# Kernel tuning notes

Measured on AMD Instinct MI355X. Metric: run time of the kernel, lower is better.

The kernel has to match this reference:

```python
import jax, jax.numpy as jnp
import numpy as np

T, B, F, P = 1024, 2048, 11, 256
KAPPA_MAX = 0.1
N_GRID = 100


def setup_inputs() -> dict:
    key = jax.random.key(0)
    k1, k2, k3, k4, k5 = jax.random.split(key, 5)
    aidx = jax.random.randint(k1, (T, B), 0, 2)
    actions = jax.nn.one_hot(aidx, 2, dtype=jnp.float32)            # (T,B,2) one-hot choice
    rewards = jax.random.bernoulli(k2, 0.5, (T, B, 2)).astype(jnp.float32)
    cd_cur = jax.random.uniform(k3, (T, B, 1), minval=-0.1, maxval=0.1)
    cd_next = jax.random.uniform(k4, (T, B, 1), minval=-0.1, maxval=0.1)
    meta = jnp.zeros((T, B, 4), dtype=jnp.float32)                  # timestep/trial/block/experiment (unused)
    pid = jax.random.randint(k5, (B,), 0, P).astype(jnp.float32)
    pid_feat = jnp.broadcast_to(pid[None, :, None], (T, B, 1))
    inputs = jnp.concatenate([actions, rewards, cd_cur, cd_next, meta, pid_feat], axis=-1)
    inputs = inputs[:, None]                                        # (T, 1, B, 11)
    return {
        "inputs": inputs,
        "beta_raw": jnp.zeros((P,), dtype=jnp.float32),
        "sigma_raw": jnp.zeros((P,), dtype=jnp.float32),
    }


def reference(inputs, beta_raw, sigma_raw):
    p_mu = jnp.linspace(0.0, 1.0, N_GRID)                           # (100,)
    x = jnp.nan_to_num(inputs[:, 0])                                # (T, B, 11)
    pid = x[0, :, -1].astype(jnp.int32)                             # (B,)
    beta = jnp.clip(jax.nn.softplus(beta_raw) + 1.0, 1.0, 25.0)[pid]    # (B,)
    sigma = jnp.clip(jax.nn.sigmoid(sigma_raw) * 0.09 + 0.01, 0.01, 0.1)[pid]  # (B,)
    inv_s = 1.0 / (sigma * jnp.sqrt(2.0))

    def ncdf(v, mean):
        return 0.5 * (1.0 + jax.lax.erf((v - mean) * inv_s))

    def state_beliefs(cd):
        u = ncdf(0.0, cd)
        v = ncdf(-KAPPA_MAX, cd)
        w = ncdf(KAPPA_MAX, cd)
        denom = jnp.maximum(w - v, 1e-10)
        pi_0 = jnp.clip((u - v) / denom, 0.0, 1.0)
        pi_1 = jnp.clip((w - u) / denom, 0.0, 1.0)
        return pi_0, pi_1

    def step(belief, x_t):
        acts = x_t[:, :2]
        rews = x_t[:, 2:4]
        cd_current = x_t[:, 4]
        cd_next = x_t[:, 5]
        had_choice = acts.sum(-1) > 0
        action_idx = jnp.argmax(acts, axis=-1)
        reward_scalar = (rews * acts).sum(-1)
        pi_0, pi_1 = state_beliefs(cd_current)
        r = jnp.where(action_idx == 0, reward_scalar, 1.0 - reward_scalar)
        q_0 = pi_1 * r + pi_0 * (1.0 - r)
        q_1 = (2.0 * r - 1.0) * (pi_0 - pi_1)
        update = q_1[:, None] * p_mu + q_0[:, None]                 # (B, 100)
        update = jnp.where(had_choice[:, None], update, 1.0)
        belief = jnp.maximum(belief * update, 1e-30)
        belief_norm = belief / belief.sum(-1, keepdims=True)
        E_mu = (belief_norm * p_mu).sum(-1)                         # (B,)
        pi_0n, pi_1n = state_beliefs(cd_next)
        v_a0 = (pi_0n - pi_1n) * E_mu + pi_1n
        v_a1 = (pi_1n - pi_0n) * E_mu + pi_0n
        logits_t = beta[:, None] * jnp.stack([v_a0, v_a1], axis=-1)  # (B, 2)
        return belief, logits_t

    belief0 = jnp.ones((x.shape[1], N_GRID), dtype=x.dtype)
    belief, logits = jax.lax.scan(step, belief0, x)                 # logits: (T, B, 2)
    logits = logits[:, None]                                        # (T, 1, B, 2)
    return logits, belief
```

## Files before the change

### kernel.cpp

```cpp
#include <hip/hip_runtime.h>
#include <math.h>

#define TT  1024
#define BB  2048
#define FF  11
#define PP  256
#define NG  100
#define NCH 16
#define LCH (TT / NCH)
#define JJ  4

typedef float f32x2 __attribute__((ext_vector_type(2)));

__device__ __forceinline__ float nz(float v) { return (v != v) ? 0.f : v; }

__device__ __forceinline__ float erf_fast(float x) {
    float ax = fabsf(x);
    float t  = __builtin_amdgcn_rcpf(fmaf(0.3275911f, ax, 1.f));
    float y  = fmaf(fmaf(fmaf(fmaf(1.061405429f, t, -1.453152027f), t,
                              1.421413741f), t, -0.284496736f), t, 0.254829592f);
    y *= t;
    float r = fmaf(-y, __expf(-ax * ax), 1.f);
    return copysignf(r, x);
}

__global__ __launch_bounds__(256) void phase1_kernel(
    const float* __restrict__ x, const float* __restrict__ beta_raw,
    const float* __restrict__ sigma_raw, float4* __restrict__ QC)
{
    __shared__ float s[256 * FF];
    const int tid = threadIdx.x;
    const size_t base = (size_t)blockIdx.x * (256 * FF);
    {
        const float4* x4 = (const float4*)(x + base);
        float4* s4 = (float4*)s;
        #pragma unroll
        for (int k = tid; k < 704; k += 256) s4[k] = x4[k];
    }
    __syncthreads();

    const int idx = blockIdx.x * 256 + tid;
    const int b   = idx & (BB - 1);
    const float* rec = s + tid * FF;
    float a0  = nz(rec[0]);
    float a1  = nz(rec[1]);
    float r0  = nz(rec[2]);
    float r1  = nz(rec[3]);
    float cdc = nz(rec[4]);
    float cdn = nz(rec[5]);

    int pid = (int)nz(x[(size_t)b * FF + 10]);
    pid = pid < 0 ? 0 : (pid > PP - 1 ? PP - 1 : pid);
    float br = beta_raw[pid];
    float sr = sigma_raw[pid];
    float sp   = fmaxf(br, 0.f) + log1pf(__expf(-fabsf(br)));
    float beta = fminf(fmaxf(sp + 1.f, 1.f), 25.f);
    float sig  = fminf(fmaxf(__builtin_amdgcn_rcpf(1.f + __expf(-sr)) * 0.09f + 0.01f,
                             0.01f), 0.1f);
    float inv_s = 1.f / (sig * 1.41421356237309505f);

    float u = 0.5f * (1.f + erf_fast((0.0f  - cdc) * inv_s));
    float v = 0.5f * (1.f + erf_fast((-0.1f - cdc) * inv_s));
    float w = 0.5f * (1.f + erf_fast((0.1f  - cdc) * inv_s));
    float inv = 1.f / fmaxf(w - v, 1e-10f);
    float pi0 = fminf(fmaxf((u - v) * inv, 0.f), 1.f);
    float pi1 = fminf(fmaxf((w - u) * inv, 0.f), 1.f);

    u = 0.5f * (1.f + erf_fast((0.0f  - cdn) * inv_s));
    v = 0.5f * (1.f + erf_fast((-0.1f - cdn) * inv_s));
    w = 0.5f * (1.f + erf_fast((0.1f  - cdn) * inv_s));
    inv = 1.f / fmaxf(w - v, 1e-10f);
    float pi0n = fminf(fmaxf((u - v) * inv, 0.f), 1.f);
    float pi1n = fminf(fmaxf((w - u) * inv, 0.f), 1.f);

    float rs = r0 * a0 + r1 * a1;
    float r  = (a0 >= a1) ? rs : 1.f - rs;
    float q0 = pi1 * r + pi0 * (1.f - r);
    float q1 = (2.f * r - 1.f) * (pi0 - pi1);
    if (!((a0 + a1) > 0.f)) { q0 = 1.f; q1 = 0.f; }

    QC[idx] = make_float4(q0, q1, beta * pi1n, beta * pi0n);
}

template <int CTRL, int RMASK>
__device__ __forceinline__ float dpp_add(float v) {
    int t = __builtin_amdgcn_update_dpp(0, __float_as_int(v), CTRL, RMASK, 0xF, true);
    return v + __int_as_float(t);
}
__device__ __forceinline__ float red8(float v) {
    v = dpp_add<0xB1,  0xF>(v);
    v = dpp_add<0x4E,  0xF>(v);
    v = dpp_add<0x141, 0xF>(v);
    return v;
}


__global__ __launch_bounds__(256) void phaseA_kernel(
    const float4* __restrict__ QC, float2* __restrict__ UC)
{
    const int lane = threadIdx.x & 63;
    const int wib  = threadIdx.x >> 6;
    const int W    = blockIdx.x * 4 + wib;
    const int pair = W & 1023;
    const int c    = W >> 10;
    const int lig  = lane & 31;
    const int b    = 2 * pair + (lane >> 5);
    const int t0   = c * LCH;

    const f32x2 p01 = { (float)lig        * (1.f / 99.f),
                        (float)(lig + 32) * (1.f / 99.f) };
    const f32x2 p23 = { (float)(lig + 64) * (1.f / 99.f),
                        (float)(lig + 96) * (1.f / 99.f) };
    const f32x2 cl01 = { 1e-30f, 1e-30f };
    const f32x2 cl23 = { 1e-30f, (lig < 4) ? 1e-30f : 0.f };

    f32x2 U01 = { 1.f, 1.f }, U23 = { 1.f, 1.f };
    f32x2 C01 = { 0.f, 0.f }, C23 = { 0.f, 0.f };

    const char* QCb = (const char*)QC;
    unsigned off = ((unsigned)t0 * BB + (unsigned)b) * 16u;

    float4 pre[JJ];
    #pragma unroll
    for (int j = 0; j < JJ; ++j)
        pre[j] = *(const float4*)(QCb + (off + (unsigned)j * (BB * 16u)));
    off += JJ * (BB * 16u);

    for (int tt = 0; tt < LCH; tt += JJ) {
        #pragma unroll
        for (int j = 0; j < JJ; ++j) {
            float4 q = pre[j];
            pre[j] = *(const float4*)(QCb + (off + (unsigned)j * (BB * 16u)));
            f32x2 qx = { q.x, q.x }, qy = { q.y, q.y };
            f32x2 u01 = qy * p01 + qx;
            f32x2 u23 = qy * p23 + qx;
            U01 *= u01;
            U23 *= u23;
            C01 = __builtin_elementwise_max(C01 * u01, cl01);
            C23 = __builtin_elementwise_max(C23 * u23, cl23);
        }
        off += JJ * (BB * 16u);
    }

    float2* dst = UC + ((size_t)c * BB + b) * NG;
    dst[lig]      = make_float2(U01.x, C01.x);
    dst[lig + 32] = make_float2(U01.y, C01.y);
    dst[lig + 64] = make_float2(U23.x, C23.x);
    if (lig < 4) dst[lig + 96] = make_float2(U23.y, C23.y);
}

__global__ __launch_bounds__(256) void phaseB_kernel(
    const float2* __restrict__ UC, float* __restrict__ BE)
{
    const int flat = blockIdx.x * 256 + threadIdx.x;
    float be = 1.f;
    #pragma unroll
    for (int c = 0; c < NCH; ++c) {
        BE[(size_t)c * (BB * NG) + flat] = be;
        float2 uc = UC[(size_t)c * (BB * NG) + flat];
        be = fmaxf(be * uc.x, uc.y);
    }
}

__global__ __launch_bounds__(256) void phaseC_kernel(
    const float4* __restrict__ QC, const float* __restrict__ BE,
    float* __restrict__ out)
{
    const int lane = threadIdx.x & 63;
    const int wib  = threadIdx.x >> 6;
    const int W    = blockIdx.x * 4 + wib;
    const int wg   = W & 255;
    const int c    = W >> 8;
    const int sl   = lane & 7;
    const int g    = lane >> 3;
    const int b    = wg * 8 + g;
    const int t0   = c * LCH;

    f32x2 p[7];
    #pragma unroll
    for (int k = 0; k < 7; ++k)
        p[k] = (f32x2){ (float)(sl + 16 * k)     * (1.f / 99.f),
                        (float)(sl + 16 * k + 8) * (1.f / 99.f) };
    const f32x2 clA = { 1e-30f, 1e-30f };
    const f32x2 cl6 = { (sl < 4) ? 1e-30f : 0.f, 0.f };

    const float* ebase = BE + (size_t)c * (BB * NG) + (size_t)b * NG;
    f32x2 be[7];
    #pragma unroll
    for (int k = 0; k < 6; ++k)
        be[k] = (f32x2){ ebase[sl + 16 * k], ebase[sl + 16 * k + 8] };
    be[6] = (f32x2){ (sl < 4) ? ebase[sl + 96] : 0.f, 0.f };

    const char* QCb = (const char*)QC;
    char* outb = (char*)out;
    unsigned off  = ((unsigned)t0 * BB + (unsigned)b) * 16u;
    unsigned soff = ((unsigned)t0 * (2 * BB) + 2 * (unsigned)b) * 4u;

    float4 pre[JJ];
    #pragma unroll
    for (int j = 0; j < JJ; ++j)
        pre[j] = *(const float4*)(QCb + (off + (unsigned)j * (BB * 16u)));
    off += JJ * (BB * 16u);

    for (int tt = 0; tt < LCH; tt += JJ) {
        float S[JJ], Sp[JJ], Zv[JJ], Wv[JJ];
        #pragma unroll
        for (int j = 0; j < JJ; ++j) {
            float4 q = pre[j];
            pre[j] = *(const float4*)(QCb + (off + (unsigned)j * (BB * 16u)));
            f32x2 qx = { q.x, q.x }, qy = { q.y, q.y };
            #pragma unroll
            for (int k = 0; k < 7; ++k) {
                f32x2 u = qy * p[k] + qx;
                be[k] = __builtin_elementwise_max(be[k] * u,
                                                  (k == 6) ? cl6 : clA);
            }
            f32x2 sA = ((be[0] + be[1]) + (be[2] + be[3]))
                     + ((be[4] + be[5]) + be[6]);
            S[j] = sA.x + sA.y;
            f32x2 a1 = be[0] * p[0], a2 = be[1] * p[1];
            a1 = be[2] * p[2] + a1;  a2 = be[3] * p[3] + a2;
            a1 = be[4] * p[4] + a1;  a2 = be[5] * p[5] + a2;
            a1 = be[6] * p[6] + a1;
            f32x2 aa = a1 + a2;
            Sp[j] = aa.x + aa.y;
            Zv[j] = q.z;
            Wv[j] = q.w;
        }
        off += JJ * (BB * 16u);
        #pragma unroll
        for (int j = 0; j < JJ; ++j) {
            float st = red8(S[j]);
            float sr = red8(Sp[j]);
            float E  = sr * __builtin_amdgcn_rcpf(st);
            float A  = Wv[j] - Zv[j];
            float l0 = fmaf(A, E, Zv[j]);
            float l1 = fmaf(-A, E, Wv[j]);
            if (sl == 0)
                *(float2*)(outb + (soff + (unsigned)j * (2 * BB * 4u))) =
                    make_float2(l0, l1);
        }
        soff += JJ * (2 * BB * 4u);
    }

    if (c == NCH - 1) {
        float* bel = out + (size_t)TT * BB * 2 + (size_t)b * NG;
        #pragma unroll
        for (int k = 0; k < 6; ++k) {
            bel[sl + 16 * k]     = be[k].x;
            bel[sl + 16 * k + 8] = be[k].y;
        }
        if (sl < 4) bel[sl + 96] = be[6].x;
    }
}

extern "C" void kernel_launch(void* const* d_in, const int* in_sizes, int n_in,
                              void* d_out, int out_size, void* d_ws, size_t ws_size,
                              hipStream_t stream)
{
    const float* x         = (const float*)d_in[0];
    const float* beta_raw  = (const float*)d_in[1];
    const float* sigma_raw = (const float*)d_in[2];
    float* out = (float*)d_out;

    char* ws = (char*)d_ws;
    float4* QC = (float4*)ws;
    float2* UC = (float2*)(ws + (size_t)TT * BB * 16);
    float*  BE = (float*) (ws + (size_t)TT * BB * 16 + (size_t)NCH * BB * NG * 8);

    phase1_kernel<<<(TT * BB) / 256, 256, 0, stream>>>(x, beta_raw, sigma_raw, QC);
    phaseA_kernel<<<(BB / 2) * NCH / 4, 256, 0, stream>>>(QC, UC);
    phaseB_kernel<<<(BB * NG) / 256, 256, 0, stream>>>(UC, BE);
    phaseC_kernel<<<(BB / 8) * NCH / 4, 256, 0, stream>>>(QC, BE, out);
}
```

Measured before the change: 217.9 us.

## Fuse per-step coefficient computation into chunk-product phase with lane shuffles

New measurement: 192.6 us. 11.6% less time.

```diff
diff --git a/kernel.cpp b/kernel.cpp
--- a/kernel.cpp
+++ b/kernel.cpp
@@ -24,30 +24,47 @@
     return copysignf(r, x);
 }
 
-__global__ __launch_bounds__(256) void phase1_kernel(
+__device__ __forceinline__ float4 q_from_rec(
+    float a0, float a1, float r0, float r1, float cdc, float cdn,
+    float beta, float inv_s)
+{
+    float u = 0.5f * (1.f + erf_fast((0.0f  - cdc) * inv_s));
+    float v = 0.5f * (1.f + erf_fast((-0.1f - cdc) * inv_s));
+    float w = 0.5f * (1.f + erf_fast((0.1f  - cdc) * inv_s));
+    float inv = 1.f / fmaxf(w - v, 1e-10f);
+    float pi0 = fminf(fmaxf((u - v) * inv, 0.f), 1.f);
+    float pi1 = fminf(fmaxf((w - u) * inv, 0.f), 1.f);
+
+    u = 0.5f * (1.f + erf_fast((0.0f  - cdn) * inv_s));
+    v = 0.5f * (1.f + erf_fast((-0.1f - cdn) * inv_s));
+    w = 0.5f * (1.f + erf_fast((0.1f  - cdn) * inv_s));
+    inv = 1.f / fmaxf(w - v, 1e-10f);
+    float pi0n = fminf(fmaxf((u - v) * inv, 0.f), 1.f);
+    float pi1n = fminf(fmaxf((w - u) * inv, 0.f), 1.f);
+
+    float rs = r0 * a0 + r1 * a1;
+    float r  = (a0 >= a1) ? rs : 1.f - rs;
+    float q0 = pi1 * r + pi0 * (1.f - r);
+    float q1 = (2.f * r - 1.f) * (pi0 - pi1);
+    if (!((a0 + a1) > 0.f)) { q0 = 1.f; q1 = 0.f; }
+    return make_float4(q0, q1, beta * pi1n, beta * pi0n);
+}
+
+
+__global__ __launch_bounds__(256) void phaseAq_kernel(
     const float* __restrict__ x, const float* __restrict__ beta_raw,
-    const float* __restrict__ sigma_raw, float4* __restrict__ QC)
-{
-    __shared__ float s[256 * FF];
-    const int tid = threadIdx.x;
-    const size_t base = (size_t)blockIdx.x * (256 * FF);
-    {
-        const float4* x4 = (const float4*)(x + base);
-        float4* s4 = (float4*)s;
-        #pragma unroll
-        for (int k = tid; k < 704; k += 256) s4[k] = x4[k];
-    }
-    __syncthreads();
-
-    const int idx = blockIdx.x * 256 + tid;
-    const int b   = idx & (BB - 1);
-    const float* rec = s + tid * FF;
-    float a0  = nz(rec[0]);
-    float a1  = nz(rec[1]);
-    float r0  = nz(rec[2]);
-    float r1  = nz(rec[3]);
-    float cdc = nz(rec[4]);
-    float cdn = nz(rec[5]);
+    const float* __restrict__ sigma_raw, float4* __restrict__ QC,
+    float2* __restrict__ UC)
+{
+    const int lane = threadIdx.x & 63;
+    const int wib  = threadIdx.x >> 6;
+    const int W    = blockIdx.x * 4 + wib;
+    const int wg   = W & 255;
+    const int c    = W >> 8;
+    const int sl   = lane & 7;
+    const int g    = lane >> 3;
+    const int b    = wg * 8 + g;
+    const int t0   = c * LCH;
 
     int pid = (int)nz(x[(size_t)b * FF + 10]);
     pid = pid < 0 ? 0 : (pid > PP - 1 ? PP - 1 : pid);
@@ -59,94 +76,64 @@
                              0.01f), 0.1f);
     float inv_s = 1.f / (sig * 1.41421356237309505f);
 
-    float u = 0.5f * (1.f + erf_fast((0.0f  - cdc) * inv_s));
-    float v = 0.5f * (1.f + erf_fast((-0.1f - cdc) * inv_s));
-    float w = 0.5f * (1.f + erf_fast((0.1f  - cdc) * inv_s));
-    float inv = 1.f / fmaxf(w - v, 1e-10f);
-    float pi0 = fminf(fmaxf((u - v) * inv, 0.f), 1.f);
-    float pi1 = fminf(fmaxf((w - u) * inv, 0.f), 1.f);
-
-    u = 0.5f * (1.f + erf_fast((0.0f  - cdn) * inv_s));
-    v = 0.5f * (1.f + erf_fast((-0.1f - cdn) * inv_s));
-    w = 0.5f * (1.f + erf_fast((0.1f  - cdn) * inv_s));
-    inv = 1.f / fmaxf(w - v, 1e-10f);
-    float pi0n = fminf(fmaxf((u - v) * inv, 0.f), 1.f);
-    float pi1n = fminf(fmaxf((w - u) * inv, 0.f), 1.f);
-
-    float rs = r0 * a0 + r1 * a1;
-    float r  = (a0 >= a1) ? rs : 1.f - rs;
-    float q0 = pi1 * r + pi0 * (1.f - r);
-    float q1 = (2.f * r - 1.f) * (pi0 - pi1);
-    if (!((a0 + a1) > 0.f)) { q0 = 1.f; q1 = 0.f; }
-
-    QC[idx] = make_float4(q0, q1, beta * pi1n, beta * pi0n);
-}
-
-template <int CTRL, int RMASK>
-__device__ __forceinline__ float dpp_add(float v) {
-    int t = __builtin_amdgcn_update_dpp(0, __float_as_int(v), CTRL, RMASK, 0xF, true);
-    return v + __int_as_float(t);
-}
-__device__ __forceinline__ float red8(float v) {
-    v = dpp_add<0xB1,  0xF>(v);
-    v = dpp_add<0x4E,  0xF>(v);
-    v = dpp_add<0x141, 0xF>(v);
-    return v;
-}
-
-
-__global__ __launch_bounds__(256) void phaseA_kernel(
-    const float4* __restrict__ QC, float2* __restrict__ UC)
-{
-    const int lane = threadIdx.x & 63;
-    const int wib  = threadIdx.x >> 6;
-    const int W    = blockIdx.x * 4 + wib;
-    const int pair = W & 1023;
-    const int c    = W >> 10;
-    const int lig  = lane & 31;
-    const int b    = 2 * pair + (lane >> 5);
-    const int t0   = c * LCH;
-
-    const f32x2 p01 = { (float)lig        * (1.f / 99.f),
-                        (float)(lig + 32) * (1.f / 99.f) };
-    const f32x2 p23 = { (float)(lig + 64) * (1.f / 99.f),
-                        (float)(lig + 96) * (1.f / 99.f) };
-    const f32x2 cl01 = { 1e-30f, 1e-30f };
-    const f32x2 cl23 = { 1e-30f, (lig < 4) ? 1e-30f : 0.f };
-
-    f32x2 U01 = { 1.f, 1.f }, U23 = { 1.f, 1.f };
-    f32x2 C01 = { 0.f, 0.f }, C23 = { 0.f, 0.f };
-
-    const char* QCb = (const char*)QC;
-    unsigned off = ((unsigned)t0 * BB + (unsigned)b) * 16u;
-
-    float4 pre[JJ];
-    #pragma unroll
-    for (int j = 0; j < JJ; ++j)
-        pre[j] = *(const float4*)(QCb + (off + (unsigned)j * (BB * 16u)));
-    off += JJ * (BB * 16u);
-
-    for (int tt = 0; tt < LCH; tt += JJ) {
-        #pragma unroll
-        for (int j = 0; j < JJ; ++j) {
-            float4 q = pre[j];
-            pre[j] = *(const float4*)(QCb + (off + (unsigned)j * (BB * 16u)));
-            f32x2 qx = { q.x, q.x }, qy = { q.y, q.y };
-            f32x2 u01 = qy * p01 + qx;
-            f32x2 u23 = qy * p23 + qx;
-            U01 *= u01;
-            U23 *= u23;
-            C01 = __builtin_elementwise_max(C01 * u01, cl01);
-            C23 = __builtin_elementwise_max(C23 * u23, cl23);
-        }
-        off += JJ * (BB * 16u);
+    f32x2 p[7];
+    #pragma unroll
+    for (int k = 0; k < 7; ++k)
+        p[k] = (f32x2){ (float)(sl + 16 * k)     * (1.f / 99.f),
+                        (float)(sl + 16 * k + 8) * (1.f / 99.f) };
+    const f32x2 clA = { 1e-30f, 1e-30f };
+    const f32x2 cl6 = { (sl < 4) ? 1e-30f : 0.f, 0.f };
+
+    f32x2 U[7], C[7];
+    #pragma unroll
+    for (int k = 0; k < 7; ++k) { U[k] = (f32x2){1.f, 1.f}; C[k] = (f32x2){0.f, 0.f}; }
+
+    const float* rp = x + ((size_t)(t0 + sl) * BB + b) * FF;
+    float4 qc;
+    {
+        float a0 = nz(rp[0]), a1 = nz(rp[1]), r0 = nz(rp[2]),
+              r1 = nz(rp[3]), dc = nz(rp[4]), dn = nz(rp[5]);
+        qc = q_from_rec(a0, a1, r0, r1, dc, dn, beta, inv_s);
+        QC[(size_t)(t0 + sl) * BB + b] = qc;
+    }
+
+    for (int tt = 0; tt < LCH; tt += 8) {
+        const bool have = (tt + 8) < LCH;
+        float na0, na1, nr0, nr1, ndc, ndn;
+        if (have) {
+            const float* np = x + ((size_t)(t0 + tt + 8 + sl) * BB + b) * FF;
+            na0 = nz(np[0]); na1 = nz(np[1]); nr0 = nz(np[2]);
+            nr1 = nz(np[3]); ndc = nz(np[4]); ndn = nz(np[5]);
+        }
+        float q0b[8], q1b[8];
+        #pragma unroll
+        for (int j = 0; j < 8; ++j) {
+            q0b[j] = __shfl(qc.x, (lane & 56) + j);
+            q1b[j] = __shfl(qc.y, (lane & 56) + j);
+        }
+        #pragma unroll
+        for (int j = 0; j < 8; ++j) {
+            f32x2 qx = { q0b[j], q0b[j] }, qy = { q1b[j], q1b[j] };
+            #pragma unroll
+            for (int k = 0; k < 7; ++k) {
+                f32x2 u = qy * p[k] + qx;
+                U[k] *= u;
+                C[k] = __builtin_elementwise_max(C[k] * u, (k == 6) ? cl6 : clA);
+            }
+        }
+        if (have) {
+            qc = q_from_rec(na0, na1, nr0, nr1, ndc, ndn, beta, inv_s);
+            QC[(size_t)(t0 + tt + 8 + sl) * BB + b] = qc;
+        }
     }
 
     float2* dst = UC + ((size_t)c * BB + b) * NG;
-    dst[lig]      = make_float2(U01.x, C01.x);
-    dst[lig + 32] = make_float2(U01.y, C01.y);
-    dst[lig + 64] = make_float2(U23.x, C23.x);
-    if (lig < 4) dst[lig + 96] = make_float2(U23.y, C23.y);
+    #pragma unroll
+    for (int k = 0; k < 6; ++k) {
+        dst[sl + 16 * k]     = make_float2(U[k].x, C[k].x);
+        dst[sl + 16 * k + 8] = make_float2(U[k].y, C[k].y);
+    }
+    if (sl < 4) dst[sl + 96] = make_float2(U[6].x, C[6].x);
 }
 
 __global__ __launch_bounds__(256) void phaseB_kernel(
@@ -230,8 +217,22 @@
         off += JJ * (BB * 16u);
         #pragma unroll
         for (int j = 0; j < JJ; ++j) {
-            float st = red8(S[j]);
-            float sr = red8(Sp[j]);
+            float st = S[j], sr = Sp[j];
+            {
+                int t;
+                t = __builtin_amdgcn_update_dpp(0, __float_as_int(st), 0xB1, 0xF, 0xF, true);
+                st += __int_as_float(t);
+                t = __builtin_amdgcn_update_dpp(0, __float_as_int(sr), 0xB1, 0xF, 0xF, true);
+                sr += __int_as_float(t);
+                t = __builtin_amdgcn_update_dpp(0, __float_as_int(st), 0x4E, 0xF, 0xF, true);
+                st += __int_as_float(t);
+                t = __builtin_amdgcn_update_dpp(0, __float_as_int(sr), 0x4E, 0xF, 0xF, true);
+                sr += __int_as_float(t);
+                t = __builtin_amdgcn_update_dpp(0, __float_as_int(st), 0x141, 0xF, 0xF, true);
+                st += __int_as_float(t);
+                t = __builtin_amdgcn_update_dpp(0, __float_as_int(sr), 0x141, 0xF, 0xF, true);
+                sr += __int_as_float(t);
+            }
             float E  = sr * __builtin_amdgcn_rcpf(st);
             float A  = Wv[j] - Zv[j];
             float l0 = fmaf(A, E, Zv[j]);
@@ -268,8 +269,7 @@
     float2* UC = (float2*)(ws + (size_t)TT * BB * 16);
     float*  BE = (float*) (ws + (size_t)TT * BB * 16 + (size_t)NCH * BB * NG * 8);
 
-    phase1_kernel<<<(TT * BB) / 256, 256, 0, stream>>>(x, beta_raw, sigma_raw, QC);
-    phaseA_kernel<<<(BB / 2) * NCH / 4, 256, 0, stream>>>(QC, UC);
+    phaseAq_kernel<<<(BB / 8) * NCH / 4, 256, 0, stream>>>(x, beta_raw, sigma_raw, QC, UC);
     phaseB_kernel<<<(BB * NG) / 256, 256, 0, stream>>>(UC, BE);
     phaseC_kernel<<<(BB / 8) * NCH / 4, 256, 0, stream>>>(QC, BE, out);
 }
```
